# Performance work log

Measured on AMD Instinct MI355X. Metric: run time of the kernel, lower is better.

## Reference

```python
import jax, jax.numpy as jnp
import numpy as np
from jax import lax

R = 2            # search_range
S = 2 * R + 1    # window extent per axis
NCH = S ** 3     # output channels (125)


def _offset_table():
    # Loop order matches the original triple loop (i over H, j over W, h over D).
    # Channel index (S*i + S*j + h) may be negative -> Python negative indexing,
    starts, chans = [], []
    for i in range(-R, R + 1):          # H shift
        for j in range(-R, R + 1):      # W shift
            for h in range(-R, R + 1):  # D shift
                # out[a] = sum_c x1[a] * x2[a - shift]; padded start = R - shift
                starts.append((R - h, R - i, R - j))
                chans.append((S * i + S * j + h) % NCH)
    src = np.full(NCH, -1, dtype=np.int64)
    for t, c in enumerate(chans):
        src[c] = t
    return np.asarray(starts, np.int32), src


def setup_inputs() -> dict:
    key = jax.random.key(0)
    k1, k2 = jax.random.split(key)
    B, C, D, H, W = 2, 64, 32, 64, 64
    x1 = jax.random.normal(k1, (B, C, D, H, W), dtype=jnp.float32)
    x2 = jax.random.normal(k2, (B, C, D, H, W), dtype=jnp.float32)
    return {"x1": x1, "x2": x2}


def reference(x1, x2):
    B, C, D, H, W = x1.shape
    starts_np, src_np = _offset_table()
    starts = jnp.asarray(starts_np)                          # [NCH, 3]
    # zero-pad x2 so every shifted window is a static-size slice
    x2p = jnp.pad(x2, ((0, 0), (0, 0), (R, R), (R, R), (R, R)))

    def corr(off):
        x2s = lax.dynamic_slice(x2p, (0, 0, off[0], off[1], off[2]),
                                (B, C, D, H, W))
        return jnp.einsum('bcdhw,bcdhw->bdhw', x1, x2s)

    corrs = lax.map(corr, starts)                            # [NCH, B, D, H, W]
    src = jnp.asarray(src_np)
    written = (src >= 0)[:, None, None, None, None]
    cv = jnp.where(written, corrs[jnp.clip(src, 0)], jnp.float32(0.0))
    return jnp.transpose(cv, (1, 0, 2, 3, 4)) / NCH          # [B, NCH, D, H, W]
```

## Files before the change

### kernel.cpp

```cpp
#include <hip/hip_runtime.h>

#define B_ 2
#define C_ 64
#define D_ 32
#define H_ 64
#define W_ 64
#define NCH 125
#define HW_ 4096
#define DHW_ 131072
#define CDHW_ 8388608

#define TROWS 12
#define TBUF (TROWS * W_)

typedef float f32x4 __attribute__((ext_vector_type(4)));

__device__ __attribute__((aligned(16))) const float g_zero[4] = {0.f, 0.f, 0.f, 0.f};

__device__ __forceinline__ void glds16(const float* g, float* l) {
    __builtin_amdgcn_global_load_lds(
        (const __attribute__((address_space(1))) void*)g,
        (__attribute__((address_space(3))) void*)l, 16, 0, 0);
}

__device__ __forceinline__ void nt_store4(float* p, float a, float b,
                                          float c, float d) {
    f32x4 v = {a, b, c, d};
    __builtin_nontemporal_store(v, (f32x4*)p);
}

__global__ __launch_bounds__(128, 5) void cv_all(const float* __restrict__ x1,
                                                 const float* __restrict__ x2,
                                                 float* __restrict__ out)
{
    __shared__ __align__(16) float lds[4 + 3 * TBUF + 4];

    const int tid  = threadIdx.y * 16 + threadIdx.x;
    const int lane = tid & 63;
    const int w    = tid >> 6;
    const int tx   = lane & 15;
    const int lr0  = lane >> 4;

    const int lin     = blockIdx.x;
    const int logical = (lin & 7) * 320 + (lin >> 3);
    const int bz   = logical % 10;
    const int rest = logical / 10;
    const int y0   = (rest & 7) * 8;
    const int d    = rest >> 3;
    const int b    = bz / 5;
    const int hi   = bz - b * 5;
    const int hh   = hi - 2;
    const int y    = y0 + 4 * w + lr0;
    const int x    = tx * 4;
    const int zd   = d - hh;
    const bool zok = (zd >= 0) && (zd < D_);

    const int q   = lane & 15;
    const int rr  = lane >> 4;
    const int rowA = (w == 0) ? (y0 - 2 + rr) : (y0 + 6 + rr);
    const int rowB = y0 + 2 + rr;
    const bool vA = zok && (rowA >= 0) && (rowA < H_);
    const bool vB = zok;
    const float* x2b = x2 + (size_t)b * CDHW_ + (size_t)(zok ? zd : 0) * HW_;
    const float* pA = vA ? (x2b + rowA * W_ + 4 * q) : g_zero;
    const float* pB = vB ? (x2b + rowB * W_ + 4 * q) : g_zero;
    const int sA = vA ? DHW_ : 0;
    const int sB = vB ? DHW_ : 0;
    const int dof = w ? 512 : 0;

    const float* p1 = x1 + (size_t)b * CDHW_ + (size_t)d * HW_ + (y * W_ + x);

    glds16(pA, lds + 4 + dof);
    if (w == 0) glds16(pB, lds + 4 + 256);
    float4 a0 = *(const float4*)p1;
    pA += sA; pB += sB;

    float acc[9][4];
#pragma unroll
    for (int k = 0; k < 9; ++k)
#pragma unroll
        for (int j = 0; j < 4; ++j) acc[k][j] = 0.f;

    const bool lo_edge = (tx == 0);
    const bool hi_edge = (tx == 15);
    const int  t0      = 4 * w + lr0;

#pragma unroll 2
    for (int c = 0; c < C_; ++c) {
        float* dst = lds + 4 + ((c + 1) % 3) * TBUF;
        glds16(pA, dst + dof);
        if (w == 0) glds16(pB, dst + 256);
        float4 a1 = *(const float4*)(p1 + (size_t)((c + 1) & 63) * DHW_);
        if (c < 62) { pA += sA; pB += sB; }

        if (w == 0) asm volatile("s_waitcnt vmcnt(3)" ::: "memory");
        else        asm volatile("s_waitcnt vmcnt(2)" ::: "memory");
        __builtin_amdgcn_s_barrier();
        __builtin_amdgcn_sched_barrier(0);

        const float* Bb = lds + 4 + (c % 3) * TBUF;
        const float4 a = a0;
        float2 k0A, k0B;
#pragma unroll
        for (int k = 0; k < 5; ++k) {
            const float* pr = Bb + (t0 + k) * W_ + x;
            const float2 cA = *(const float2*)(pr + 2);
            float2 cB = *(const float2*)(pr + 4);
            cB.x = hi_edge ? 0.f : cB.x;
            cB.y = hi_edge ? 0.f : cB.y;
            if (k == 0) { k0A = cA; k0B = cB; }
            const int ai = 4 - k;
            acc[ai][0] += a.x * cA.x;
            acc[ai][1] += a.y * cA.y;
            acc[ai][2] += a.z * cB.x;
            acc[ai][3] += a.w * cB.y;
        }
        {
            const float* pr = Bb + t0 * W_ + x;
            float2 rlA = *(const float2*)(pr - 2);
            const float2 rlB = *(const float2*)(pr);
            rlA.x = lo_edge ? 0.f : rlA.x;
            rlA.y = lo_edge ? 0.f : rlA.y;
            const float r8[8] = {rlA.x, rlA.y, rlB.x, rlB.y,
                                 k0A.x, k0A.y, k0B.x, k0B.y};
#pragma unroll
            for (int s = 1; s <= 4; ++s) {
                const int ai = s + 4;
                acc[ai][0] += a.x * r8[4 - s];
                acc[ai][1] += a.y * r8[5 - s];
                acc[ai][2] += a.z * r8[6 - s];
                acc[ai][3] += a.w * r8[7 - s];
            }
        }
        a0 = a1;
    }

    float* ob = out + (size_t)b * NCH * DHW_ + (size_t)d * HW_ + (y * W_ + x);
    const float inv = 1.0f / 125.0f;
#pragma unroll
    for (int k = 0; k < 9; ++k) {
        const int s = k - 4;
        int ch = 5 * s + hh;
        ch = (ch % NCH + NCH) % NCH;
        nt_store4(ob + (size_t)ch * DHW_,
                  acc[k][0] * inv, acc[k][1] * inv,
                  acc[k][2] * inv, acc[k][3] * inv);
    }
}

extern "C" void kernel_launch(void* const* d_in, const int* in_sizes, int n_in,
                              void* d_out, int out_size, void* d_ws, size_t ws_size,
                              hipStream_t stream) {
    const float* x1 = (const float*)d_in[0];
    const float* x2 = (const float*)d_in[1];
    float* out = (float*)d_out;
    cv_all<<<dim3(2560, 1, 1), dim3(16, 8, 1), 0, stream>>>(x1, x2, out);
}
```

Measured before the change: 239.8 us.

## Process two channels per barrier with double-buffered LDS slabs loaded per wave

The pipeline moves from a triple-buffered, one-channel-per-iteration scheme to a double-buffered scheme. Each iteration stages two channels, and each wave loads the full 12-row slab for its own channel. This halves the number of barriers and waitcnt stalls, and the load work is split evenly between the two waves. In exchange, LDS use grows (2x1536 floats instead of 3x768), which could lower occupancy. The vmcnt(0) wait also drains all outstanding loads before each barrier, so load latency is less hidden.

```diff
diff --git a/kernel.cpp b/kernel.cpp
--- a/kernel.cpp
+++ b/kernel.cpp
@@ -10,8 +10,8 @@
 #define DHW_ 131072
 #define CDHW_ 8388608
 
-#define TROWS 12
-#define TBUF (TROWS * W_)
+#define SLAB 768
+#define BUFSZ (2 * SLAB)
 
 typedef float f32x4 __attribute__((ext_vector_type(4)));
 
@@ -33,7 +33,7 @@
                                                  const float* __restrict__ x2,
                                                  float* __restrict__ out)
 {
-    __shared__ __align__(16) float lds[4 + 3 * TBUF + 4];
+    __shared__ __align__(16) float lds[4 + 2 * BUFSZ + 4];
 
     const int tid  = threadIdx.y * 16 + threadIdx.x;
     const int lane = tid & 63;
@@ -55,25 +55,32 @@
     const int zd   = d - hh;
     const bool zok = (zd >= 0) && (zd < D_);
 
-    const int q   = lane & 15;
-    const int rr  = lane >> 4;
-    const int rowA = (w == 0) ? (y0 - 2 + rr) : (y0 + 6 + rr);
-    const int rowB = y0 + 2 + rr;
-    const bool vA = zok && (rowA >= 0) && (rowA < H_);
-    const bool vB = zok;
-    const float* x2b = x2 + (size_t)b * CDHW_ + (size_t)(zok ? zd : 0) * HW_;
-    const float* pA = vA ? (x2b + rowA * W_ + 4 * q) : g_zero;
-    const float* pB = vB ? (x2b + rowB * W_ + 4 * q) : g_zero;
-    const int sA = vA ? DHW_ : 0;
-    const int sB = vB ? DHW_ : 0;
-    const int dof = w ? 512 : 0;
+    const int q  = lane & 15;
+    const int rr = lane >> 4;
+    const float* x2b = x2 + (size_t)b * CDHW_ + (size_t)w * DHW_
+                          + (size_t)(zok ? zd : 0) * HW_;
+    const float* pG[3];
+    int sG[3];
+#pragma unroll
+    for (int G = 0; G < 3; ++G) {
+        const int grow = y0 - 2 + 4 * G + rr;
+        const bool v = zok && (grow >= 0) && (grow < H_);
+        pG[G] = v ? (x2b + grow * W_ + 4 * q) : g_zero;
+        sG[G] = v ? 2 * DHW_ : 0;
+    }
 
     const float* p1 = x1 + (size_t)b * CDHW_ + (size_t)d * HW_ + (y * W_ + x);
 
-    glds16(pA, lds + 4 + dof);
-    if (w == 0) glds16(pB, lds + 4 + 256);
+    {
+        float* dst = lds + 4 + w * SLAB;
+        glds16(pG[0], dst);
+        glds16(pG[1], dst + 256);
+        glds16(pG[2], dst + 512);
+    }
     float4 a0 = *(const float4*)p1;
-    pA += sA; pB += sB;
+    float4 a1 = *(const float4*)(p1 + DHW_);
+#pragma unroll
+    for (int G = 0; G < 3; ++G) pG[G] += sG[G];
 
     float acc[9][4];
 #pragma unroll
@@ -86,53 +93,63 @@
     const int  t0      = 4 * w + lr0;
 
 #pragma unroll 2
-    for (int c = 0; c < C_; ++c) {
-        float* dst = lds + 4 + ((c + 1) % 3) * TBUF;
-        glds16(pA, dst + dof);
-        if (w == 0) glds16(pB, dst + 256);
-        float4 a1 = *(const float4*)(p1 + (size_t)((c + 1) & 63) * DHW_);
-        if (c < 62) { pA += sA; pB += sB; }
-
-        if (w == 0) asm volatile("s_waitcnt vmcnt(3)" ::: "memory");
-        else        asm volatile("s_waitcnt vmcnt(2)" ::: "memory");
+    for (int i = 0; i < 32; ++i) {
+        asm volatile("s_waitcnt vmcnt(0)" ::: "memory");
         __builtin_amdgcn_s_barrier();
         __builtin_amdgcn_sched_barrier(0);
 
-        const float* Bb = lds + 4 + (c % 3) * TBUF;
-        const float4 a = a0;
-        float2 k0A, k0B;
+        {
+            float* dst = lds + 4 + ((i + 1) & 1) * BUFSZ + w * SLAB;
+            glds16(pG[0], dst);
+            glds16(pG[1], dst + 256);
+            glds16(pG[2], dst + 512);
+        }
+        float4 na0 = *(const float4*)(p1 + (size_t)((2 * i + 2) & 63) * DHW_);
+        float4 na1 = *(const float4*)(p1 + (size_t)((2 * i + 3) & 63) * DHW_);
+        if (i < 30) {
 #pragma unroll
-        for (int k = 0; k < 5; ++k) {
-            const float* pr = Bb + (t0 + k) * W_ + x;
-            const float2 cA = *(const float2*)(pr + 2);
-            float2 cB = *(const float2*)(pr + 4);
-            cB.x = hi_edge ? 0.f : cB.x;
-            cB.y = hi_edge ? 0.f : cB.y;
-            if (k == 0) { k0A = cA; k0B = cB; }
-            const int ai = 4 - k;
-            acc[ai][0] += a.x * cA.x;
-            acc[ai][1] += a.y * cA.y;
-            acc[ai][2] += a.z * cB.x;
-            acc[ai][3] += a.w * cB.y;
+            for (int G = 0; G < 3; ++G) pG[G] += sG[G];
         }
-        {
-            const float* pr = Bb + t0 * W_ + x;
-            float2 rlA = *(const float2*)(pr - 2);
-            const float2 rlB = *(const float2*)(pr);
-            rlA.x = lo_edge ? 0.f : rlA.x;
-            rlA.y = lo_edge ? 0.f : rlA.y;
-            const float r8[8] = {rlA.x, rlA.y, rlB.x, rlB.y,
-                                 k0A.x, k0A.y, k0B.x, k0B.y};
+
+        const float* Bb = lds + 4 + (i & 1) * BUFSZ;
 #pragma unroll
-            for (int s = 1; s <= 4; ++s) {
-                const int ai = s + 4;
-                acc[ai][0] += a.x * r8[4 - s];
-                acc[ai][1] += a.y * r8[5 - s];
-                acc[ai][2] += a.z * r8[6 - s];
-                acc[ai][3] += a.w * r8[7 - s];
+        for (int s2 = 0; s2 < 2; ++s2) {
+            const float* Bs = Bb + s2 * SLAB;
+            const float4 a = s2 ? a1 : a0;
+            float2 k0A, k0B;
+#pragma unroll
+            for (int k = 0; k < 5; ++k) {
+                const float* pr = Bs + (t0 + k) * W_ + x;
+                const float2 cA = *(const float2*)(pr + 2);
+                float2 cB = *(const float2*)(pr + 4);
+                cB.x = hi_edge ? 0.f : cB.x;
+                cB.y = hi_edge ? 0.f : cB.y;
+                if (k == 0) { k0A = cA; k0B = cB; }
+                const int ai = 4 - k;
+                acc[ai][0] += a.x * cA.x;
+                acc[ai][1] += a.y * cA.y;
+                acc[ai][2] += a.z * cB.x;
+                acc[ai][3] += a.w * cB.y;
+            }
+            {
+                const float* pr = Bs + t0 * W_ + x;
+                float2 rlA = *(const float2*)(pr - 2);
+                const float2 rlB = *(const float2*)(pr);
+                rlA.x = lo_edge ? 0.f : rlA.x;
+                rlA.y = lo_edge ? 0.f : rlA.y;
+                const float r8[8] = {rlA.x, rlA.y, rlB.x, rlB.y,
+                                     k0A.x, k0A.y, k0B.x, k0B.y};
+#pragma unroll
+                for (int s = 1; s <= 4; ++s) {
+                    const int ai = s + 4;
+                    acc[ai][0] += a.x * r8[4 - s];
+                    acc[ai][1] += a.y * r8[5 - s];
+                    acc[ai][2] += a.z * r8[6 - s];
+                    acc[ai][3] += a.w * r8[7 - s];
+                }
             }
         }
-        a0 = a1;
+        a0 = na0; a1 = na1;
     }
 
     float* ob = out + (size_t)b * NCH * DHW_ + (size_t)d * HW_ + (y * W_ + x);
```

Result: no change. 239.4 us, median of 3 (-0.2%).
